# Kernel tuning notes

Hardware: AMD Instinct MI355X
Metric: run time of the kernel (lower is better)

The kernel has to match this reference:

```python
import jax, jax.numpy as jnp
import numpy as np

NUM_BANDS = 64
LATENT = 256
HIDDEN = 512
G = 8
K = 1024
GD = LATENT // G  # 32
BETA = 0.25


def setup_inputs() -> dict:
    key = jax.random.key(0)
    ks = jax.random.split(key, 10)
    B, T = 16, 1000
    bands = jax.random.normal(ks[0], (B, T, NUM_BANDS), dtype=jnp.float32)
    s = 0.02
    enc_w1 = jax.random.normal(ks[1], (NUM_BANDS, HIDDEN), dtype=jnp.float32) * s
    enc_b1 = jnp.zeros((HIDDEN,), dtype=jnp.float32)
    enc_w2 = jax.random.normal(ks[2], (HIDDEN, LATENT), dtype=jnp.float32) * s
    enc_b2 = jnp.zeros((LATENT,), dtype=jnp.float32)
    codebooks = jax.random.normal(ks[3], (G, K, GD), dtype=jnp.float32) * 0.1
    dec_w1 = jax.random.normal(ks[4], (LATENT, HIDDEN), dtype=jnp.float32) * s
    dec_b1 = jnp.zeros((HIDDEN,), dtype=jnp.float32)
    dec_w2 = jax.random.normal(ks[5], (HIDDEN, NUM_BANDS), dtype=jnp.float32) * s
    dec_b2 = jnp.zeros((NUM_BANDS,), dtype=jnp.float32)
    return {
        "bands": bands,
        "enc_w1": enc_w1, "enc_b1": enc_b1, "enc_w2": enc_w2, "enc_b2": enc_b2,
        "codebooks": codebooks,
        "dec_w1": dec_w1, "dec_b1": dec_b1, "dec_w2": dec_w2, "dec_b2": dec_b2,
    }


def _mlp(x, w1, b1, w2, b2):
    # TimeDistributedMLP: Linear -> ReLU -> Linear applied on last dim
    return jax.nn.relu(x @ w1 + b1) @ w2 + b2


def reference(bands, enc_w1, enc_b1, enc_w2, enc_b2, codebooks,
              dec_w1, dec_b1, dec_w2, dec_b2):
    B, T, _ = bands.shape
    z_e = _mlp(bands, enc_w1, enc_b1, enc_w2, enc_b2)  # (B,T,LATENT)

    # Grouped VQ over flattened frames
    parts = z_e.reshape(B * T, G, GD)                   # (N,G,gd)
    zn = jnp.sum(parts * parts, axis=-1)[:, :, None]    # (N,G,1)
    cn = jnp.sum(codebooks * codebooks, axis=-1)[None]  # (1,G,K)
    cross = jnp.einsum('ngd,gkd->ngk', parts, codebooks)
    dist = zn - 2.0 * cross + cn                        # (N,G,K)
    idx = jnp.argmin(dist, axis=-1)                     # (N,G) int
    z_q = codebooks[jnp.arange(G)[None, :], idx]        # (N,G,gd) gather

    # straight-through estimator
    z_q_st = parts + jax.lax.stop_gradient(z_q - parts)

    # per-group mean losses, summed over groups
    codebook_loss = jnp.sum(jnp.mean((jax.lax.stop_gradient(z_q) - parts) ** 2, axis=(0, 2)))
    commit_loss = jnp.sum(jnp.mean((z_q - jax.lax.stop_gradient(parts)) ** 2, axis=(0, 2)))
    vq_loss = BETA * (codebook_loss + commit_loss)  # epoch=None -> beta_eff = beta

    z_q_out = z_q_st.reshape(B, T, LATENT)
    idx_out = idx.reshape(B, T, G)
    bands_hat = _mlp(z_q_out, dec_w1, dec_b1, dec_w2, dec_b2)
    return (bands_hat, z_e, z_q_out, idx_out, vq_loss)
```

## Files before the change

### kernel.cpp

```cpp
#include <hip/hip_runtime.h>

#define NBANDS 64
#define LATENT 256
#define HIDDEN 512
#define GQ 8
#define KQ 1024
#define GD 32
#define NROWS 16000

#define OUT_BH   0
#define OUT_ZE   1024000
#define OUT_ZQ   5120000
#define OUT_IDX  9216000
#define OUT_LOSS 9344000

#define WS_H     0
#define WS_H2BF_F  0
#define WS_ZQB_F   4096000
#define WS_W1B_F   6144000
#define WS_W2B_F   6209536
#define WS_CBH_F   6240000
#define WS_CBM_F   6400000
#define WS_CBL_F   6560000
#define WS_CN    8192000
#define WS_LOSS  8200192

typedef __attribute__((ext_vector_type(8))) short bf16x8;
typedef __attribute__((ext_vector_type(4))) float f32x4;

__device__ __forceinline__ unsigned short f2bf(float f) {
  unsigned u = __builtin_bit_cast(unsigned, f);
  unsigned r = u + 0x7FFFu + ((u >> 16) & 1u);
  return (unsigned short)(r >> 16);
}

__device__ __forceinline__ float bf2f(unsigned short h) {
  return __builtin_bit_cast(float, ((unsigned)h) << 16);
}

__device__ __forceinline__ void split3(float x, unsigned short& h,
                                       unsigned short& m, unsigned short& l) {
  h = f2bf(x);
  const float r1 = x - bf2f(h);
  m = f2bf(r1);
  const float r2 = r1 - bf2f(m);
  l = f2bf(r2);
}

template<int BN, int TM, int TN, int BK, bool RELU>
__global__ __launch_bounds__(256) void gemm_f32(
    const float* __restrict__ A, const float* __restrict__ B,
    const float* __restrict__ bias, float* __restrict__ C,
    int M, int N, int K) {
  constexpr int BM = 128;
  constexpr int NTX = BN / TN;
  constexpr int AF4 = BK / 8;
  constexpr int QPR = BN / 4;
  constexpr int BF4 = BK * BN / 1024;

  __shared__ float As[BK][BM + 8];
  __shared__ float Bs[BK][BN + 4];

  const int tid = threadIdx.x;
  const int tx = tid % NTX;
  const int ty = tid / NTX;
  const int row0 = blockIdx.y * BM;
  const int col0 = blockIdx.x * BN;

  const int arow = tid >> 1;
  const int akq  = (tid & 1) * (BK / 2);

  float acc[TM][TN] = {};

  for (int k0 = 0; k0 < K; k0 += BK) {
    float4 av[AF4], bv[BF4];
#pragma unroll
    for (int q = 0; q < AF4; ++q)
      av[q] = *reinterpret_cast<const float4*>(
          &A[(size_t)(row0 + arow) * K + k0 + akq + q * 4]);
#pragma unroll
    for (int t = 0; t < BF4; ++t) {
      const int qq = tid * BF4 + t;
      const int bk = qq / QPR, bn4 = qq % QPR;
      bv[t] = *reinterpret_cast<const float4*>(
          &B[(size_t)(k0 + bk) * N + col0 + bn4 * 4]);
    }
    __syncthreads();
#pragma unroll
    for (int q = 0; q < AF4; ++q) {
      As[akq + q * 4 + 0][arow] = av[q].x;
      As[akq + q * 4 + 1][arow] = av[q].y;
      As[akq + q * 4 + 2][arow] = av[q].z;
      As[akq + q * 4 + 3][arow] = av[q].w;
    }
#pragma unroll
    for (int t = 0; t < BF4; ++t) {
      const int qq = tid * BF4 + t;
      const int bk = qq / QPR, bn4 = qq % QPR;
      *reinterpret_cast<float4*>(&Bs[bk][bn4 * 4]) = bv[t];
    }
    __syncthreads();

#pragma unroll
    for (int kk = 0; kk < BK; ++kk) {
      float a[TM], b[TN];
#pragma unroll
      for (int q = 0; q < TM / 4; ++q) {
        float4 v = *reinterpret_cast<const float4*>(&As[kk][ty * TM + q * 4]);
        a[q * 4 + 0] = v.x; a[q * 4 + 1] = v.y;
        a[q * 4 + 2] = v.z; a[q * 4 + 3] = v.w;
      }
#pragma unroll
      for (int q = 0; q < TN / 4; ++q) {
        float4 v = *reinterpret_cast<const float4*>(&Bs[kk][tx * TN + q * 4]);
        b[q * 4 + 0] = v.x; b[q * 4 + 1] = v.y;
        b[q * 4 + 2] = v.z; b[q * 4 + 3] = v.w;
      }
#pragma unroll
      for (int i = 0; i < TM; ++i)
#pragma unroll
        for (int j = 0; j < TN; ++j)
          acc[i][j] = fmaf(a[i], b[j], acc[i][j]);
    }
  }

  float bb[TN];
#pragma unroll
  for (int q = 0; q < TN / 4; ++q) {
    float4 v = *reinterpret_cast<const float4*>(&bias[col0 + tx * TN + q * 4]);
    bb[q * 4 + 0] = v.x; bb[q * 4 + 1] = v.y;
    bb[q * 4 + 2] = v.z; bb[q * 4 + 3] = v.w;
  }
#pragma unroll
  for (int i = 0; i < TM; ++i) {
    const int r = row0 + ty * TM + i;
#pragma unroll
    for (int q = 0; q < TN / 4; ++q) {
      float4 v;
      float* vp = &v.x;
#pragma unroll
      for (int j = 0; j < 4; ++j) {
        float t = acc[i][q * 4 + j] + bb[q * 4 + j];
        if (RELU) t = fmaxf(t, 0.0f);
        vp[j] = t;
      }
      *reinterpret_cast<float4*>(&C[(size_t)r * N + col0 + tx * TN + q * 4]) = v;
    }
  }
}

template<int WM, bool OUT_BF16, bool DO_LOSS>
__global__ __launch_bounds__(256) void gemm_bf16_mfma(
    const unsigned short* __restrict__ A, const unsigned short* __restrict__ BT,
    const float* __restrict__ bias, void* __restrict__ Cout,
    int M, int N, int K,
    const float* __restrict__ loss_acc, float* __restrict__ loss_out) {
  constexpr int BM = 4 * WM;
  constexpr int MT = WM / 16;

  __shared__ unsigned short As[BM][40];
  __shared__ unsigned short Bs[64][40];

  const int tid  = threadIdx.x;
  const int wave = tid >> 6;
  const int lane = tid & 63;
  const int quad = lane >> 4;
  const int l16  = lane & 15;
  const int row0 = blockIdx.y * BM;
  const int col0 = blockIdx.x * 64;

  if (DO_LOSS && blockIdx.x == 0 && blockIdx.y == 0 && tid == 0)
    loss_out[0] = 0.5f * loss_acc[0] / (float)((size_t)NROWS * GD);

  f32x4 acc[MT][4];
#pragma unroll
  for (int mt = 0; mt < MT; ++mt)
#pragma unroll
    for (int nt = 0; nt < 4; ++nt) acc[mt][nt] = (f32x4){0.f, 0.f, 0.f, 0.f};

  for (int k0 = 0; k0 < K; k0 += 32) {
    __syncthreads();
    if constexpr (BM == 128) {
      const int r = tid >> 1, seg = (tid & 1) * 16;
      const uint4* src = reinterpret_cast<const uint4*>(
          &A[(size_t)(row0 + r) * K + k0 + seg]);
      uint4* dst = reinterpret_cast<uint4*>(&As[r][seg]);
      dst[0] = src[0]; dst[1] = src[1];
    } else {
      const int r = tid >> 2, seg = (tid & 3) * 8;
      *reinterpret_cast<uint4*>(&As[r][seg]) =
          *reinterpret_cast<const uint4*>(&A[(size_t)(row0 + r) * K + k0 + seg]);
    }
    {
      const int n = tid >> 2, kc = (tid & 3) * 8;
      *reinterpret_cast<uint4*>(&Bs[n][kc]) =
          *reinterpret_cast<const uint4*>(&BT[(size_t)(col0 + n) * K + k0 + kc]);
    }
    __syncthreads();

    bf16x8 af[MT], bf[4];
#pragma unroll
    for (int mt = 0; mt < MT; ++mt)
      af[mt] = *reinterpret_cast<const bf16x8*>(
          &As[wave * WM + mt * 16 + l16][quad * 8]);
#pragma unroll
    for (int nt = 0; nt < 4; ++nt)
      bf[nt] = *reinterpret_cast<const bf16x8*>(&Bs[nt * 16 + l16][quad * 8]);
#pragma unroll
    for (int mt = 0; mt < MT; ++mt)
#pragma unroll
      for (int nt = 0; nt < 4; ++nt)
        acc[mt][nt] = __builtin_amdgcn_mfma_f32_16x16x32_bf16(
            af[mt], bf[nt], acc[mt][nt], 0, 0, 0);
  }

#pragma unroll
  for (int mt = 0; mt < MT; ++mt)
#pragma unroll
    for (int nt = 0; nt < 4; ++nt) {
      const int col = col0 + nt * 16 + l16;
      const float bv = bias[col];
#pragma unroll
      for (int r = 0; r < 4; ++r) {
        const int grow = row0 + wave * WM + mt * 16 + quad * 4 + r;
        float v = acc[mt][nt][r] + bv;
        if constexpr (OUT_BF16) {
          v = fmaxf(v, 0.0f);
          ((unsigned short*)Cout)[(size_t)grow * N + col] = f2bf(v);
        } else {
          ((float*)Cout)[(size_t)grow * N + col] = v;
        }
      }
    }
}

__global__ void prep_cn(const float* __restrict__ cb, float* __restrict__ cn,
                        float* __restrict__ loss_acc) {
  const int i = blockIdx.x * 256 + threadIdx.x;
  if (i == 0) loss_acc[0] = 0.0f;
  if (i < GQ * KQ) {
    const float* c = cb + (size_t)i * GD;
    float s = 0.0f;
#pragma unroll
    for (int d = 0; d < GD; ++d) s = fmaf(c[d], c[d], s);
    cn[i] = -0.5f * s;
  }
}

__global__ void prep_wT(const float* __restrict__ w1, const float* __restrict__ w2,
                        const float* __restrict__ cbk,
                        unsigned short* __restrict__ w1bT,
                        unsigned short* __restrict__ w2bT,
                        unsigned short* __restrict__ cbh,
                        unsigned short* __restrict__ cbm,
                        unsigned short* __restrict__ cbl) {
  const int t = blockIdx.x * 256 + threadIdx.x;
  if (t < 16384) {
    const int n = t >> 5, k0 = (t & 31) * 8;
    alignas(16) unsigned short o[8];
#pragma unroll
    for (int q = 0; q < 8; ++q) o[q] = f2bf(w1[(size_t)(k0 + q) * HIDDEN + n]);
    *reinterpret_cast<uint4*>(&w1bT[(size_t)n * LATENT + k0]) =
        *reinterpret_cast<const uint4*>(o);
  } else if (t < 20480) {
    const int u = t - 16384;
    const int n = u >> 6, k0 = (u & 63) * 8;
    alignas(16) unsigned short o[8];
#pragma unroll
    for (int q = 0; q < 8; ++q) o[q] = f2bf(w2[(size_t)(k0 + q) * NBANDS + n]);
    *reinterpret_cast<uint4*>(&w2bT[(size_t)n * HIDDEN + k0]) =
        *reinterpret_cast<const uint4*>(o);
  } else if (t < 53248) {
    const int e0 = (t - 20480) * 8;
    alignas(16) unsigned short oh[8], om[8], ol[8];
#pragma unroll
    for (int q = 0; q < 8; ++q) split3(cbk[e0 + q], oh[q], om[q], ol[q]);
    *reinterpret_cast<uint4*>(&cbh[e0]) = *reinterpret_cast<const uint4*>(oh);
    *reinterpret_cast<uint4*>(&cbm[e0]) = *reinterpret_cast<const uint4*>(om);
    *reinterpret_cast<uint4*>(&cbl[e0]) = *reinterpret_cast<const uint4*>(ol);
  }
}

__global__ __launch_bounds__(256) void vq_mfma(
    const float* __restrict__ z_e, const float* __restrict__ cb,
    const float* __restrict__ cnh,
    const unsigned short* __restrict__ cbh,
    const unsigned short* __restrict__ cbm,
    const unsigned short* __restrict__ cbl,
    float* __restrict__ z_q, unsigned short* __restrict__ zqb,
    float* __restrict__ idx_out, float* __restrict__ loss_acc) {
  const int g    = blockIdx.y;
  const int row0 = blockIdx.x * 128;
  const int tid  = threadIdx.x;
  const int wave = tid >> 6;
  const int lane = tid & 63;
  const int quad = lane >> 4;
  const int l16  = lane & 15;

  bf16x8 ah[2], am[2], al[2];
#pragma unroll
  for (int mt = 0; mt < 2; ++mt) {
    const float* zp = &z_e[(size_t)(row0 + wave * 32 + mt * 16 + l16) * LATENT
                           + g * GD + quad * 8];
    const float4 x0 = *reinterpret_cast<const float4*>(zp);
    const float4 x1 = *reinterpret_cast<const float4*>(zp + 4);
    const float xv[8] = {x0.x, x0.y, x0.z, x0.w, x1.x, x1.y, x1.z, x1.w};
    bf16x8 vh, vm, vl;
#pragma unroll
    for (int j = 0; j < 8; ++j) {
      unsigned short sh, sm, sl;
      split3(xv[j], sh, sm, sl);
      vh[j] = (short)sh; vm[j] = (short)sm; vl[j] = (short)sl;
    }
    ah[mt] = vh; am[mt] = vm; al[mt] = vl;
  }

  const size_t cb0 = (size_t)g * KQ * GD;
  const float* cng = cnh + g * KQ;

  float best[8];
  int   bidx[8];
#pragma unroll
  for (int i = 0; i < 8; ++i) { best[i] = -3.0e38f; bidx[i] = 0; }

#pragma unroll 2
  for (int ch = 0; ch < 16; ++ch) {
#pragma unroll
    for (int nt = 0; nt < 4; ++nt) {
      const int code = ch * 64 + nt * 16 + l16;
      const size_t cba = cb0 + (size_t)code * GD + quad * 8;
      const bf16x8 bh = *reinterpret_cast<const bf16x8*>(&cbh[cba]);
      const bf16x8 bm = *reinterpret_cast<const bf16x8*>(&cbm[cba]);
      const bf16x8 bl = *reinterpret_cast<const bf16x8*>(&cbl[cba]);
      const float c0 = cng[code];
      f32x4 a0 = {c0, c0, c0, c0};
      f32x4 a1 = a0;
      a0 = __builtin_amdgcn_mfma_f32_16x16x32_bf16(ah[0], bh, a0, 0, 0, 0);
      a1 = __builtin_amdgcn_mfma_f32_16x16x32_bf16(ah[1], bh, a1, 0, 0, 0);
      a0 = __builtin_amdgcn_mfma_f32_16x16x32_bf16(ah[0], bm, a0, 0, 0, 0);
      a1 = __builtin_amdgcn_mfma_f32_16x16x32_bf16(ah[1], bm, a1, 0, 0, 0);
      a0 = __builtin_amdgcn_mfma_f32_16x16x32_bf16(am[0], bh, a0, 0, 0, 0);
      a1 = __builtin_amdgcn_mfma_f32_16x16x32_bf16(am[1], bh, a1, 0, 0, 0);
      a0 = __builtin_amdgcn_mfma_f32_16x16x32_bf16(ah[0], bl, a0, 0, 0, 0);
      a1 = __builtin_amdgcn_mfma_f32_16x16x32_bf16(ah[1], bl, a1, 0, 0, 0);
      a0 = __builtin_amdgcn_mfma_f32_16x16x32_bf16(am[0], bm, a0, 0, 0, 0);
      a1 = __builtin_amdgcn_mfma_f32_16x16x32_bf16(am[1], bm, a1, 0, 0, 0);
      a0 = __builtin_amdgcn_mfma_f32_16x16x32_bf16(al[0], bh, a0, 0, 0, 0);
      a1 = __builtin_amdgcn_mfma_f32_16x16x32_bf16(al[1], bh, a1, 0, 0, 0);
#pragma unroll
      for (int r = 0; r < 4; ++r) {
        if (a0[r] > best[r])     { best[r] = a0[r];     bidx[r] = code; }
        if (a1[r] > best[4 + r]) { best[4 + r] = a1[r]; bidx[4 + r] = code; }
      }
    }
  }

  float sse_local = 0.0f;
#pragma unroll
  for (int s8 = 0; s8 < 8; ++s8) {
    float mb = best[s8];
    int   mi = bidx[s8];
#pragma unroll
    for (int m = 1; m < 16; m <<= 1) {
      const float ov = __shfl_xor(mb, m, 64);
      const int   oi = __shfl_xor(mi, m, 64);
      if (ov > mb || (ov == mb && oi < mi)) { mb = ov; mi = oi; }
    }
    const int mt  = s8 >> 2;
    const int r   = s8 & 3;
    const int row = row0 + wave * 32 + mt * 16 + quad * 4 + r;
    const float2 cw = *reinterpret_cast<const float2*>(
        &cb[cb0 + (size_t)mi * GD + 2 * l16]);
    const float2 zv = *reinterpret_cast<const float2*>(
        &z_e[(size_t)row * LATENT + g * GD + 2 * l16]);
    const float d0 = cw.x - zv.x;
    const float d1 = cw.y - zv.y;
    sse_local = fmaf(d0, d0, fmaf(d1, d1, sse_local));
    *reinterpret_cast<float2*>(
        &z_q[(size_t)row * LATENT + g * GD + 2 * l16]) = cw;
    const unsigned pz = (unsigned)f2bf(cw.x) | ((unsigned)f2bf(cw.y) << 16);
    *reinterpret_cast<unsigned*>(
        &zqb[(size_t)row * LATENT + g * GD + 2 * l16]) = pz;
    if (l16 == 0) idx_out[(size_t)row * GQ + g] = (float)mi;
  }

#pragma unroll
  for (int m = 1; m < 64; m <<= 1) sse_local += __shfl_xor(sse_local, m, 64);
  if (lane == 0) atomicAdd(loss_acc, sse_local);
}

extern "C" void kernel_launch(void* const* d_in, const int* in_sizes, int n_in,
                              void* d_out, int out_size, void* d_ws, size_t ws_size,
                              hipStream_t stream) {
  const float* bands  = (const float*)d_in[0];
  const float* enc_w1 = (const float*)d_in[1];
  const float* enc_b1 = (const float*)d_in[2];
  const float* enc_w2 = (const float*)d_in[3];
  const float* enc_b2 = (const float*)d_in[4];
  const float* cbooks = (const float*)d_in[5];
  const float* dec_w1 = (const float*)d_in[6];
  const float* dec_b1 = (const float*)d_in[7];
  const float* dec_w2 = (const float*)d_in[8];
  const float* dec_b2 = (const float*)d_in[9];

  float* out = (float*)d_out;
  float* ws  = (float*)d_ws;

  float* bands_hat = out + OUT_BH;
  float* z_e       = out + OUT_ZE;
  float* z_q       = out + OUT_ZQ;
  float* idx_f     = out + OUT_IDX;
  float* loss_out  = out + OUT_LOSS;

  float* H        = ws + WS_H;
  float* cn       = ws + WS_CN;
  float* loss_acc = ws + WS_LOSS;
  unsigned short* h2bf = (unsigned short*)(ws + WS_H2BF_F);
  unsigned short* zqb  = (unsigned short*)(ws + WS_ZQB_F);
  unsigned short* w1bT = (unsigned short*)(ws + WS_W1B_F);
  unsigned short* w2bT = (unsigned short*)(ws + WS_W2B_F);
  unsigned short* cbh  = (unsigned short*)(ws + WS_CBH_F);
  unsigned short* cbm  = (unsigned short*)(ws + WS_CBM_F);
  unsigned short* cbl  = (unsigned short*)(ws + WS_CBL_F);

  prep_cn<<<dim3(32), dim3(256), 0, stream>>>(cbooks, cn, loss_acc);

  gemm_f32<128, 8, 8, 16, true ><<<dim3(HIDDEN / 128, NROWS / 128), dim3(256), 0, stream>>>(
      bands, enc_w1, enc_b1, H, NROWS, HIDDEN, NBANDS);
  gemm_f32<64, 4, 8, 32, false><<<dim3(LATENT / 64, NROWS / 128), dim3(256), 0, stream>>>(
      H, enc_w2, enc_b2, z_e, NROWS, LATENT, HIDDEN);

  prep_wT<<<dim3(208), dim3(256), 0, stream>>>(
      dec_w1, dec_w2, cbooks, w1bT, w2bT, cbh, cbm, cbl);

  vq_mfma<<<dim3(NROWS / 128, GQ), dim3(256), 0, stream>>>(
      z_e, cbooks, cn, cbh, cbm, cbl, z_q, zqb, idx_f, loss_acc);

  gemm_bf16_mfma<32, true, true ><<<dim3(HIDDEN / 64, NROWS / 128), dim3(256), 0, stream>>>(
      zqb, w1bT, dec_b1, (void*)h2bf, NROWS, HIDDEN, LATENT, loss_acc, loss_out);
  gemm_bf16_mfma<16, false, false><<<dim3(NBANDS / 64, NROWS / 64), dim3(256), 0, stream>>>(
      h2bf, w2bT, dec_b2, (void*)bands_hat, NROWS, NBANDS, HIDDEN, loss_acc, loss_out);
}
```

Before: 304.7 us.

## Stage VQ codebook chunks through double-buffered LDS with register prefetch

The VQ argmin kernel now loads each 64-code chunk of the hi/mid/lo bf16 codebook splits and code norms cooperatively into a double-buffered shared-memory tile. The next chunk is prefetched into registers while the current one is computed. Two code tiles are interleaved per step so more independent MFMAs are in flight. This replaces per-wave redundant global loads, which every one of the four waves issued, with one shared load per block. The cost is about 25KB of LDS per block, extra barriers, more register pressure, and a launch-bounds occupancy hint.

```diff
diff --git a/kernel.cpp b/kernel.cpp
--- a/kernel.cpp
+++ b/kernel.cpp
@@ -281,7 +281,89 @@
   }
 }
 
-__global__ __launch_bounds__(256) void vq_mfma(
+struct VqStg { uint4 h, m, l; float c; };
+
+__device__ __forceinline__ void vq_ldg(
+    VqStg& s, const unsigned short* __restrict__ cbh,
+    const unsigned short* __restrict__ cbm,
+    const unsigned short* __restrict__ cbl,
+    const float* __restrict__ cng, int gsh, int ch, int tid) {
+  const int o = gsh + ch * 2048 + tid * 8;
+  s.h = *reinterpret_cast<const uint4*>(&cbh[o]);
+  s.m = *reinterpret_cast<const uint4*>(&cbm[o]);
+  s.l = *reinterpret_cast<const uint4*>(&cbl[o]);
+  if (tid < 64) s.c = cng[ch * 64 + tid];
+}
+
+__device__ __forceinline__ void vq_stl(
+    unsigned short (&buf)[6272], const VqStg& s, int tid) {
+  *reinterpret_cast<uint4*>(&buf[tid * 8])        = s.h;
+  *reinterpret_cast<uint4*>(&buf[2048 + tid * 8]) = s.m;
+  *reinterpret_cast<uint4*>(&buf[4096 + tid * 8]) = s.l;
+  if (tid < 64) *reinterpret_cast<float*>(&buf[6144 + tid * 2]) = s.c;
+}
+
+__device__ __forceinline__ void vq_pair(
+    const bf16x8 (&ah)[2], const bf16x8 (&am)[2], const bf16x8 (&al)[2],
+    const unsigned short (&buf)[6272], int laneoff, int nt0, int ch, int l16,
+    float (&best)[8], int (&bidx)[8]) {
+  bf16x8 Fh[2], Fm[2], Fl[2];
+  float  Fc[2];
+#pragma unroll
+  for (int p = 0; p < 2; ++p) {
+    const int off = laneoff + (nt0 + p) * 512;
+    Fh[p] = *reinterpret_cast<const bf16x8*>(&buf[off]);
+    Fm[p] = *reinterpret_cast<const bf16x8*>(&buf[2048 + off]);
+    Fl[p] = *reinterpret_cast<const bf16x8*>(&buf[4096 + off]);
+    Fc[p] = *reinterpret_cast<const float*>(&buf[6144 + (((nt0 + p) * 16 + l16) << 1)]);
+  }
+  f32x4 a00 = {Fc[0], Fc[0], Fc[0], Fc[0]};
+  f32x4 a01 = a00;
+  f32x4 a10 = {Fc[1], Fc[1], Fc[1], Fc[1]};
+  f32x4 a11 = a10;
+  a00 = __builtin_amdgcn_mfma_f32_16x16x32_bf16(ah[0], Fh[0], a00, 0, 0, 0);
+  a01 = __builtin_amdgcn_mfma_f32_16x16x32_bf16(ah[1], Fh[0], a01, 0, 0, 0);
+  a10 = __builtin_amdgcn_mfma_f32_16x16x32_bf16(ah[0], Fh[1], a10, 0, 0, 0);
+  a11 = __builtin_amdgcn_mfma_f32_16x16x32_bf16(ah[1], Fh[1], a11, 0, 0, 0);
+  a00 = __builtin_amdgcn_mfma_f32_16x16x32_bf16(ah[0], Fm[0], a00, 0, 0, 0);
+  a01 = __builtin_amdgcn_mfma_f32_16x16x32_bf16(ah[1], Fm[0], a01, 0, 0, 0);
+  a10 = __builtin_amdgcn_mfma_f32_16x16x32_bf16(ah[0], Fm[1], a10, 0, 0, 0);
+  a11 = __builtin_amdgcn_mfma_f32_16x16x32_bf16(ah[1], Fm[1], a11, 0, 0, 0);
+  a00 = __builtin_amdgcn_mfma_f32_16x16x32_bf16(am[0], Fh[0], a00, 0, 0, 0);
+  a01 = __builtin_amdgcn_mfma_f32_16x16x32_bf16(am[1], Fh[0], a01, 0, 0, 0);
+  a10 = __builtin_amdgcn_mfma_f32_16x16x32_bf16(am[0], Fh[1], a10, 0, 0, 0);
+  a11 = __builtin_amdgcn_mfma_f32_16x16x32_bf16(am[1], Fh[1], a11, 0, 0, 0);
+  a00 = __builtin_amdgcn_mfma_f32_16x16x32_bf16(ah[0], Fl[0], a00, 0, 0, 0);
+  a01 = __builtin_amdgcn_mfma_f32_16x16x32_bf16(ah[1], Fl[0], a01, 0, 0, 0);
+  a10 = __builtin_amdgcn_mfma_f32_16x16x32_bf16(ah[0], Fl[1], a10, 0, 0, 0);
+  a11 = __builtin_amdgcn_mfma_f32_16x16x32_bf16(ah[1], Fl[1], a11, 0, 0, 0);
+  a00 = __builtin_amdgcn_mfma_f32_16x16x32_bf16(am[0], Fm[0], a00, 0, 0, 0);
+  a01 = __builtin_amdgcn_mfma_f32_16x16x32_bf16(am[1], Fm[0], a01, 0, 0, 0);
+  a10 = __builtin_amdgcn_mfma_f32_16x16x32_bf16(am[0], Fm[1], a10, 0, 0, 0);
+  a11 = __builtin_amdgcn_mfma_f32_16x16x32_bf16(am[1], Fm[1], a11, 0, 0, 0);
+  a00 = __builtin_amdgcn_mfma_f32_16x16x32_bf16(al[0], Fh[0], a00, 0, 0, 0);
+  a01 = __builtin_amdgcn_mfma_f32_16x16x32_bf16(al[1], Fh[0], a01, 0, 0, 0);
+  a10 = __builtin_amdgcn_mfma_f32_16x16x32_bf16(al[0], Fh[1], a10, 0, 0, 0);
+  a11 = __builtin_amdgcn_mfma_f32_16x16x32_bf16(al[1], Fh[1], a11, 0, 0, 0);
+  {
+    const int code = ch * 64 + nt0 * 16 + l16;
+#pragma unroll
+    for (int r = 0; r < 4; ++r) {
+      if (a00[r] > best[r])     { best[r]     = a00[r]; bidx[r]     = code; }
+      if (a01[r] > best[4 + r]) { best[4 + r] = a01[r]; bidx[4 + r] = code; }
+    }
+  }
+  {
+    const int code = ch * 64 + (nt0 + 1) * 16 + l16;
+#pragma unroll
+    for (int r = 0; r < 4; ++r) {
+      if (a10[r] > best[r])     { best[r]     = a10[r]; bidx[r]     = code; }
+      if (a11[r] > best[4 + r]) { best[4 + r] = a11[r]; bidx[4 + r] = code; }
+    }
+  }
+}
+
+__global__ __launch_bounds__(256, 3) void vq_mfma(
     const float* __restrict__ z_e, const float* __restrict__ cb,
     const float* __restrict__ cnh,
     const unsigned short* __restrict__ cbh,
@@ -289,6 +371,8 @@
     const unsigned short* __restrict__ cbl,
     float* __restrict__ z_q, unsigned short* __restrict__ zqb,
     float* __restrict__ idx_out, float* __restrict__ loss_acc) {
+  __shared__ __align__(16) unsigned short lds[2][6272];
+
   const int g    = blockIdx.y;
   const int row0 = blockIdx.x * 128;
   const int tid  = threadIdx.x;
@@ -297,6 +381,14 @@
   const int quad = lane >> 4;
   const int l16  = lane & 15;
 
+  const int gsh = g * (KQ * GD);
+  const float* cng = cnh + g * KQ;
+  const size_t cb0 = (size_t)g * KQ * GD;
+  const int laneoff = l16 * 32 + quad * 8;
+
+  VqStg sX, sY;
+  vq_ldg(sX, cbh, cbm, cbl, cng, gsh, 0, tid);
+
   bf16x8 ah[2], am[2], al[2];
 #pragma unroll
   for (int mt = 0; mt < 2; ++mt) {
@@ -315,43 +407,31 @@
     ah[mt] = vh; am[mt] = vm; al[mt] = vl;
   }
 
-  const size_t cb0 = (size_t)g * KQ * GD;
-  const float* cng = cnh + g * KQ;
-
   float best[8];
   int   bidx[8];
 #pragma unroll
   for (int i = 0; i < 8; ++i) { best[i] = -3.0e38f; bidx[i] = 0; }
 
-#pragma unroll 2
-  for (int ch = 0; ch < 16; ++ch) {
-#pragma unroll
-    for (int nt = 0; nt < 4; ++nt) {
-      const int code = ch * 64 + nt * 16 + l16;
-      const size_t cba = cb0 + (size_t)code * GD + quad * 8;
-      const bf16x8 bh = *reinterpret_cast<const bf16x8*>(&cbh[cba]);
-      const bf16x8 bm = *reinterpret_cast<const bf16x8*>(&cbm[cba]);
-      const bf16x8 bl = *reinterpret_cast<const bf16x8*>(&cbl[cba]);
-      const float c0 = cng[code];
-      f32x4 a0 = {c0, c0, c0, c0};
-      f32x4 a1 = a0;
-      a0 = __builtin_amdgcn_mfma_f32_16x16x32_bf16(ah[0], bh, a0, 0, 0, 0);
-      a1 = __builtin_amdgcn_mfma_f32_16x16x32_bf16(ah[1], bh, a1, 0, 0, 0);
-      a0 = __builtin_amdgcn_mfma_f32_16x16x32_bf16(ah[0], bm, a0, 0, 0, 0);
-      a1 = __builtin_amdgcn_mfma_f32_16x16x32_bf16(ah[1], bm, a1, 0, 0, 0);
-      a0 = __builtin_amdgcn_mfma_f32_16x16x32_bf16(am[0], bh, a0, 0, 0, 0);
-      a1 = __builtin_amdgcn_mfma_f32_16x16x32_bf16(am[1], bh, a1, 0, 0, 0);
-      a0 = __builtin_amdgcn_mfma_f32_16x16x32_bf16(ah[0], bl, a0, 0, 0, 0);
-      a1 = __builtin_amdgcn_mfma_f32_16x16x32_bf16(ah[1], bl, a1, 0, 0, 0);
-      a0 = __builtin_amdgcn_mfma_f32_16x16x32_bf16(am[0], bm, a0, 0, 0, 0);
-      a1 = __builtin_amdgcn_mfma_f32_16x16x32_bf16(am[1], bm, a1, 0, 0, 0);
-      a0 = __builtin_amdgcn_mfma_f32_16x16x32_bf16(al[0], bh, a0, 0, 0, 0);
-      a1 = __builtin_amdgcn_mfma_f32_16x16x32_bf16(al[1], bh, a1, 0, 0, 0);
-#pragma unroll
-      for (int r = 0; r < 4; ++r) {
-        if (a0[r] > best[r])     { best[r] = a0[r];     bidx[r] = code; }
-        if (a1[r] > best[4 + r]) { best[4 + r] = a1[r]; bidx[4 + r] = code; }
-      }
+  vq_stl(lds[0], sX, tid);
+  vq_ldg(sY, cbh, cbm, cbl, cng, gsh, 1, tid);
+  __syncthreads();
+
+#pragma unroll 1
+  for (int cp = 0; cp < 8; ++cp) {
+    const int ch = 2 * cp;
+    if (ch < 14) vq_ldg(sX, cbh, cbm, cbl, cng, gsh, ch + 2, tid);
+    vq_pair(ah, am, al, lds[0], laneoff, 0, ch, l16, best, bidx);
+    vq_pair(ah, am, al, lds[0], laneoff, 2, ch, l16, best, bidx);
+    vq_stl(lds[1], sY, tid);
+    __syncthreads();
+
+    const int ch2 = ch + 1;
+    if (ch2 < 14) vq_ldg(sY, cbh, cbm, cbl, cng, gsh, ch2 + 2, tid);
+    vq_pair(ah, am, al, lds[1], laneoff, 0, ch2, l16, best, bidx);
+    vq_pair(ah, am, al, lds[1], laneoff, 2, ch2, l16, best, bidx);
+    if (ch2 < 15) {
+      vq_stl(lds[0], sX, tid);
+      __syncthreads();
     }
   }
 
```

After: 320.0 us. 1.05x slower.
